# Kernel tuning notes

Hardware: AMD Instinct MI355X
Metric: run time of the kernel (lower is better)

Reference implementation:

```python
import jax, jax.numpy as jnp
import numpy as np

K = 512          # num_embeddings
D = 64           # embedding_dim
BETA = 0.25      # commitment_cost
DECAY = 0.99
EPS = 1e-5


def setup_inputs() -> dict:
    key = jax.random.key(0)
    k1, k2, k3 = jax.random.split(key, 3)
    inputs = jax.random.normal(k1, (64, D, 32, 32), dtype=jnp.float32)  # NCHW, C == embedding_dim
    embedding = jax.random.normal(k2, (K, D), dtype=jnp.float32)
    ema_w = jax.random.normal(k3, (K, D), dtype=jnp.float32)
    ema_cluster_size = jnp.zeros((K,), dtype=jnp.float32)
    return {"inputs": inputs, "embedding": embedding, "ema_w": ema_w,
            "ema_cluster_size": ema_cluster_size}


def reference(inputs, embedding, ema_w, ema_cluster_size):
    # NCHW -> NHWC, flatten to [N, D]
    x = jnp.transpose(inputs, (0, 2, 3, 1))
    B, H, W, C = x.shape
    flat = x.reshape(-1, C)                                   # [N, D]

    # squared L2 distances to all codes: [N, K]
    d = (jnp.sum(flat * flat, axis=1, keepdims=True)
         + jnp.sum(embedding * embedding, axis=1)
         - 2.0 * flat @ embedding.T)
    idx = jnp.argmin(d, axis=1)                               # [N]

    # gather (equivalent to one-hot @ embedding, without materializing one-hot)
    quantized = embedding[idx].reshape(x.shape)               # [B,H,W,D]

    # EMA codebook update (training branch); segment sums replace encodings.T matmuls
    counts = jax.ops.segment_sum(jnp.ones_like(idx, dtype=flat.dtype), idx,
                                 num_segments=K)              # [K]
    new_cs = ema_cluster_size * DECAY + (1.0 - DECAY) * counts
    n = jnp.sum(new_cs)
    new_cs = (new_cs + EPS) / (n + K * EPS) * n               # Laplace smoothing
    dw = jax.ops.segment_sum(flat, idx, num_segments=K)       # [K, D]
    new_ema_w = ema_w * DECAY + (1.0 - DECAY) * dw
    new_embedding = new_ema_w / new_cs[:, None]

    # commitment loss + straight-through estimator
    e_latent_loss = jnp.mean((jax.lax.stop_gradient(quantized) - x) ** 2)
    loss = BETA * e_latent_loss
    quantized_st = x + jax.lax.stop_gradient(quantized - x)

    avg_probs = counts / flat.shape[0]
    perplexity = jnp.exp(-jnp.sum(avg_probs * jnp.log(avg_probs + 1e-10)))

    out_q = jnp.transpose(quantized_st, (0, 3, 1, 2))         # back to NCHW
    return (loss, out_q, perplexity, idx.reshape(B, H, W),
            new_cs, new_ema_w, new_embedding)
```

## Files before the change

kernel.cpp:

```cpp
#include <hip/hip_runtime.h>

#define K_CODES 512
#define DIM 64
#define HW 1024
#define NVEC 65536

#define O0 0
#define O1 1
#define O2 4194305
#define O3 4194306
#define O4 4259842
#define O5 4260354
#define O6 4293122

#define WS_EE  64
#define WS_CNT 1024
#define WS_DW  2048
#define WS_BP  35840
#define XSS    72

typedef __bf16 bf16x8 __attribute__((ext_vector_type(8)));
typedef float  f32x4  __attribute__((ext_vector_type(4)));

__global__ void k0_init(const float* __restrict__ emb, float* __restrict__ wsf) {
    const int b = blockIdx.x, t = threadIdx.x;
    if (b < 128) {
        wsf[WS_DW + b * 256 + t] = 0.0f;
    } else if (b == 128) {
        int* cnt = (int*)(wsf + WS_CNT);
        cnt[t] = 0; cnt[t + 256] = 0;
        if (t == 0) wsf[0] = 0.0f;
    } else if (b < 131) {
        int k = (b - 129) * 256 + t;
        const float* e = emb + k * DIM;
        float s = 0.0f;
        #pragma unroll
        for (int c = 0; c < DIM; ++c) s += e[c] * e[c];
        wsf[WS_EE + k] = s;
    } else {
        int g = (b - 131) * 256 + t;
        int j    = g & 7;
        int lane = (g >> 3) & 63;
        int ks   = (g >> 9) & 1;
        int rest = g >> 10;
        int ntg  = rest & 31;
        int s    = rest >> 5;
        int code = ntg * 16 + (lane & 15);
        int c    = ks * 32 + (lane >> 4) * 8 + j;
        float v = -2.0f * emb[code * DIM + c];
        __bf16 h0 = (__bf16)v;  float r1 = v  - (float)h0;
        __bf16 h1 = (__bf16)r1; float r2 = r1 - (float)h1;
        __bf16 hv = (s == 0) ? h0 : (s == 1 ? h1 : (__bf16)r2);
        ((__bf16*)(wsf + WS_BP))[g] = hv;
    }
}

__global__ __launch_bounds__(512, 2)
void k1_main(const float* __restrict__ in, const float* __restrict__ emb,
             float* __restrict__ out, float* __restrict__ wsf) {
    __shared__ float xs[128 * XSS];
    __shared__ float pmin[4][128];
    __shared__ int   pidx[4][128];
    __shared__ float xxs[128];
    __shared__ int   hist[K_CODES];

    const int t    = threadIdx.x;
    const int lane = t & 63;
    const int wave = t >> 6;
    const int mi2  = wave & 1;
    const int ni2  = wave >> 1;
    const int col  = lane & 15;
    const int quad = lane >> 4;

    hist[t] = 0;

    const int blk     = blockIdx.x;
    const int n_img   = blk >> 3;
    const int hw_base = (blk & 7) * 128;
    const float* xbase = in + n_img * (DIM * HW) + hw_base;

    #pragma unroll
    for (int rep = 0; rep < 16; ++rep) {
        int e = rep * 512 + t;
        int c = e >> 7, h0 = e & 127;
        xs[h0 * XSS + c] = xbase[c * HW + h0];
    }

    f32x4 acc[4][8];
    #pragma unroll
    for (int nt = 0; nt < 8; ++nt) {
        float eev = wsf[WS_EE + ni2 * 128 + nt * 16 + col];
        #pragma unroll
        for (int mi = 0; mi < 4; ++mi) {
            acc[mi][nt][0] = eev; acc[mi][nt][1] = eev;
            acc[mi][nt][2] = eev; acc[mi][nt][3] = eev;
        }
    }

    __syncthreads();

    if (t < 128) {
        float s = 0.0f;
        #pragma unroll
        for (int c = 0; c < DIM; ++c) { float v = xs[t * XSS + c]; s += v * v; }
        xxs[t] = s;
    }

    const bf16x8* bp8 = (const bf16x8*)(wsf + WS_BP);

    #pragma unroll
    for (int ks = 0; ks < 2; ++ks) {
        bf16x8 A0[4], A1[4], A2[4];
        #pragma unroll
        for (int mi = 0; mi < 4; ++mi) {
            const float* src = &xs[(mi2 * 64 + mi * 16 + col) * XSS + ks * 32 + quad * 8];
            #pragma unroll
            for (int j = 0; j < 8; ++j) {
                float v = src[j];
                __bf16 h0 = (__bf16)v;  float r1 = v  - (float)h0;
                __bf16 h1 = (__bf16)r1; float r2 = r1 - (float)h1;
                A0[mi][j] = h0; A1[mi][j] = h1; A2[mi][j] = (__bf16)r2;
            }
        }
        #pragma unroll
        for (int s = 0; s < 3; ++s) {
            bf16x8 Bv[8];
            #pragma unroll
            for (int nt = 0; nt < 8; ++nt)
                Bv[nt] = bp8[(((s * 32 + ni2 * 8 + nt) * 2 + ks) * 64) + lane];
            #pragma unroll
            for (int mi = 0; mi < 4; ++mi)
                #pragma unroll
                for (int nt = 0; nt < 8; ++nt)
                    acc[mi][nt] = __builtin_amdgcn_mfma_f32_16x16x32_bf16(A0[mi], Bv[nt], acc[mi][nt], 0, 0, 0);
            if (s < 2) {
                #pragma unroll
                for (int mi = 0; mi < 4; ++mi)
                    #pragma unroll
                    for (int nt = 0; nt < 8; ++nt)
                        acc[mi][nt] = __builtin_amdgcn_mfma_f32_16x16x32_bf16(A1[mi], Bv[nt], acc[mi][nt], 0, 0, 0);
            }
            if (s == 0) {
                #pragma unroll
                for (int mi = 0; mi < 4; ++mi)
                    #pragma unroll
                    for (int nt = 0; nt < 8; ++nt)
                        acc[mi][nt] = __builtin_amdgcn_mfma_f32_16x16x32_bf16(A2[mi], Bv[nt], acc[mi][nt], 0, 0, 0);
            }
        }
    }

    #pragma unroll
    for (int mi = 0; mi < 4; ++mi) {
        #pragma unroll
        for (int r = 0; r < 4; ++r) {
            float v  = acc[mi][0][r];
            int   bi = ni2 * 128 + col;
            #pragma unroll
            for (int nt = 1; nt < 8; ++nt) {
                float u  = acc[mi][nt][r];
                int   ui = ni2 * 128 + nt * 16 + col;
                if (u < v) { v = u; bi = ui; }
            }
            #pragma unroll
            for (int off = 1; off < 16; off <<= 1) {
                float ov = __shfl_xor(v, off);
                int   oi = __shfl_xor(bi, off);
                if (ov < v || (ov == v && oi < bi)) { v = ov; bi = oi; }
            }
            if (col == 0) {
                int row = mi2 * 64 + mi * 16 + quad * 4 + r;
                pmin[ni2][row] = v;
                pidx[ni2][row] = bi;
            }
        }
    }
    __syncthreads();

    if (t < 128) {
        float v = pmin[0][t]; int bi = pidx[0][t];
        #pragma unroll
        for (int q = 1; q < 4; ++q) {
            float u = pmin[q][t]; int ui = pidx[q][t];
            if (u < v) { v = u; bi = ui; }
        }
        pidx[0][t] = bi;
        out[O3 + blk * 128 + t] = (float)bi;
        atomicAdd(&hist[bi], 1);
        float ld = v + xxs[t];
        #pragma unroll
        for (int off = 32; off > 0; off >>= 1) ld += __shfl_down(ld, off);
        if ((t & 63) == 0) atomicAdd(wsf + 0, ld);
    }
    __syncthreads();

    {
        int v = t & 127, cq = t >> 7;
        int kv = pidx[0][v];
        const float* ew = emb + kv * DIM;
        float* oq = out + O1 + n_img * (DIM * HW) + hw_base + v;
        #pragma unroll
        for (int c = cq * 16; c < cq * 16 + 16; ++c) oq[c * HW] = ew[c];
    }

    {
        float* dw = wsf + WS_DW;
        #pragma unroll 1
        for (int v = wave * 16; v < wave * 16 + 16; ++v) {
            int kv = pidx[0][v];
            atomicAdd(&dw[kv * DIM + lane], xs[v * XSS + lane]);
        }
    }

    int* cnt = (int*)(wsf + WS_CNT);
    if (hist[t]) atomicAdd(&cnt[t], hist[t]);
}

__global__ void k2a(const float* __restrict__ ema_cs, float* __restrict__ out,
                    const float* __restrict__ wsf) {
    __shared__ float s1[512], s2[512];
    const int t = threadIdx.x;
    const int* cnt = (const int*)(wsf + WS_CNT);
    float c   = (float)cnt[t];
    float raw = 0.99f * ema_cs[t] + 0.01f * c;
    float p   = c * (1.0f / 65536.0f);
    s1[t] = raw;
    s2[t] = p * logf(p + 1e-10f);
    __syncthreads();
    for (int s = 256; s > 0; s >>= 1) {
        if (t < s) { s1[t] += s1[t + s]; s2[t] += s2[t + s]; }
        __syncthreads();
    }
    float n = s1[0];
    float smooth = (raw + 1e-5f) / (n + 512.0f * 1e-5f) * n;
    out[O4 + t] = smooth;
    if (t == 0) {
        out[O2] = expf(-s2[0]);
        out[O0] = 0.25f * wsf[0] * (1.0f / 4194304.0f);
    }
}

__global__ void k2b(const float* __restrict__ ema_w, const float* __restrict__ wsf,
                    float* __restrict__ out) {
    const int m = blockIdx.x * 256 + threadIdx.x;
    const int k = m >> 6;
    float w = 0.99f * ema_w[m] + 0.01f * wsf[WS_DW + m];
    out[O5 + m] = w;
    out[O6 + m] = w / out[O4 + k];
}

extern "C" void kernel_launch(void* const* d_in, const int* in_sizes, int n_in,
                              void* d_out, int out_size, void* d_ws, size_t ws_size,
                              hipStream_t stream) {
    const float* in     = (const float*)d_in[0];
    const float* emb    = (const float*)d_in[1];
    const float* ema_w  = (const float*)d_in[2];
    const float* ema_cs = (const float*)d_in[3];
    float* out = (float*)d_out;
    float* wsf = (float*)d_ws;

    hipLaunchKernelGGL(k0_init, dim3(515), dim3(256), 0, stream, emb, wsf);
    hipLaunchKernelGGL(k1_main, dim3(512), dim3(512), 0, stream, in, emb, out, wsf);
    hipLaunchKernelGGL(k2a,     dim3(1),   dim3(512), 0, stream, ema_cs, out, wsf);
    hipLaunchKernelGGL(k2b,     dim3(128), dim3(256), 0, stream, ema_w, wsf, out);
}
```

Baseline: 161.2 us.

## Replicate atomic accumulators, write per-block loss partials, fuse finalize kernels

Splits the dw and count accumulators into four replicas indexed by block, so atomics from different blocks land on different copies and contend less. Each block writes its loss partial to its own slot instead of doing a global float atomic. The two finalize kernels are merged into one 128-block kernel that sums the replicas and recomputes the smoothed cluster sizes per block, which drops one launch. In exchange the init kernel zeroes four times as much workspace and the finalize does more redundant reads.

```diff
diff --git a/kernel.cpp b/kernel.cpp
--- a/kernel.cpp
+++ b/kernel.cpp
@@ -4,6 +4,7 @@
 #define DIM 64
 #define HW 1024
 #define NVEC 65536
+#define NREP 4
 
 #define O0 0
 #define O1 1
@@ -13,32 +14,33 @@
 #define O5 4260354
 #define O6 4293122
 
-#define WS_EE  64
-#define WS_CNT 1024
-#define WS_DW  2048
-#define WS_BP  35840
-#define XSS    72
+#define WS_LOSS 0
+#define WS_EE   512
+#define WS_CNT  1024
+#define WS_DW   4096
+#define WS_BP   135168
+#define XSS     72
 
 typedef __bf16 bf16x8 __attribute__((ext_vector_type(8)));
 typedef float  f32x4  __attribute__((ext_vector_type(4)));
 
 __global__ void k0_init(const float* __restrict__ emb, float* __restrict__ wsf) {
     const int b = blockIdx.x, t = threadIdx.x;
-    if (b < 128) {
+    if (b < 512) {
         wsf[WS_DW + b * 256 + t] = 0.0f;
-    } else if (b == 128) {
+    } else if (b == 512) {
         int* cnt = (int*)(wsf + WS_CNT);
-        cnt[t] = 0; cnt[t + 256] = 0;
-        if (t == 0) wsf[0] = 0.0f;
-    } else if (b < 131) {
-        int k = (b - 129) * 256 + t;
+        #pragma unroll
+        for (int i = 0; i < 8; ++i) cnt[i * 256 + t] = 0;
+    } else if (b < 515) {
+        int k = (b - 513) * 256 + t;
         const float* e = emb + k * DIM;
         float s = 0.0f;
         #pragma unroll
         for (int c = 0; c < DIM; ++c) s += e[c] * e[c];
         wsf[WS_EE + k] = s;
     } else {
-        int g = (b - 131) * 256 + t;
+        int g = (b - 515) * 256 + t;
         int j    = g & 7;
         int lane = (g >> 3) & 63;
         int ks   = (g >> 9) & 1;
@@ -62,6 +64,7 @@
     __shared__ float pmin[4][128];
     __shared__ int   pidx[4][128];
     __shared__ float xxs[128];
+    __shared__ float lsum[2];
     __shared__ int   hist[K_CODES];
 
     const int t    = threadIdx.x;
@@ -75,13 +78,14 @@
     hist[t] = 0;
 
     const int blk     = blockIdx.x;
+    const int rep     = blk & (NREP - 1);
     const int n_img   = blk >> 3;
     const int hw_base = (blk & 7) * 128;
     const float* xbase = in + n_img * (DIM * HW) + hw_base;
 
     #pragma unroll
-    for (int rep = 0; rep < 16; ++rep) {
-        int e = rep * 512 + t;
+    for (int rp = 0; rp < 16; ++rp) {
+        int e = rp * 512 + t;
         int c = e >> 7, h0 = e & 127;
         xs[h0 * XSS + c] = xbase[c * HW + h0];
     }
@@ -190,9 +194,11 @@
         float ld = v + xxs[t];
         #pragma unroll
         for (int off = 32; off > 0; off >>= 1) ld += __shfl_down(ld, off);
-        if ((t & 63) == 0) atomicAdd(wsf + 0, ld);
-    }
-    __syncthreads();
+        if ((t & 63) == 0) lsum[t >> 6] = ld;
+    }
+    __syncthreads();
+
+    if (t == 0) wsf[WS_LOSS + blk] = lsum[0] + lsum[1];
 
     {
         int v = t & 127, cq = t >> 7;
@@ -204,7 +210,7 @@
     }
 
     {
-        float* dw = wsf + WS_DW;
+        float* dw = wsf + WS_DW + rep * 32768;
         #pragma unroll 1
         for (int v = wave * 16; v < wave * 16 + 16; ++v) {
             int kv = pidx[0][v];
@@ -213,40 +219,67 @@
     }
 
     int* cnt = (int*)(wsf + WS_CNT);
-    if (hist[t]) atomicAdd(&cnt[t], hist[t]);
-}
-
-__global__ void k2a(const float* __restrict__ ema_cs, float* __restrict__ out,
-                    const float* __restrict__ wsf) {
-    __shared__ float s1[512], s2[512];
+    if (hist[t]) atomicAdd(&cnt[rep * 512 + t], hist[t]);
+}
+
+__global__ void k2(const float* __restrict__ ema_cs, const float* __restrict__ ema_w,
+                   float* __restrict__ out, const float* __restrict__ wsf) {
+    __shared__ float s1[256], s2[256];
     const int t = threadIdx.x;
+    const int blk = blockIdx.x;
     const int* cnt = (const int*)(wsf + WS_CNT);
-    float c   = (float)cnt[t];
-    float raw = 0.99f * ema_cs[t] + 0.01f * c;
-    float p   = c * (1.0f / 65536.0f);
-    s1[t] = raw;
-    s2[t] = p * logf(p + 1e-10f);
-    __syncthreads();
-    for (int s = 256; s > 0; s >>= 1) {
+
+    float ca = 0.0f, cb = 0.0f;
+    #pragma unroll
+    for (int r = 0; r < NREP; ++r) {
+        ca += (float)cnt[r * 512 + t];
+        cb += (float)cnt[r * 512 + 256 + t];
+    }
+    float ra = 0.99f * ema_cs[t]       + 0.01f * ca;
+    float rb = 0.99f * ema_cs[256 + t] + 0.01f * cb;
+    float pa = ca * (1.0f / 65536.0f);
+    float pb = cb * (1.0f / 65536.0f);
+    s1[t] = ra + rb;
+    s2[t] = pa * logf(pa + 1e-10f) + pb * logf(pb + 1e-10f);
+    __syncthreads();
+    for (int s = 128; s > 0; s >>= 1) {
         if (t < s) { s1[t] += s1[t + s]; s2[t] += s2[t + s]; }
         __syncthreads();
     }
-    float n = s1[0];
-    float smooth = (raw + 1e-5f) / (n + 512.0f * 1e-5f) * n;
-    out[O4 + t] = smooth;
-    if (t == 0) {
-        out[O2] = expf(-s2[0]);
-        out[O0] = 0.25f * wsf[0] * (1.0f / 4194304.0f);
-    }
-}
-
-__global__ void k2b(const float* __restrict__ ema_w, const float* __restrict__ wsf,
-                    float* __restrict__ out) {
-    const int m = blockIdx.x * 256 + threadIdx.x;
-    const int k = m >> 6;
-    float w = 0.99f * ema_w[m] + 0.01f * wsf[WS_DW + m];
-    out[O5 + m] = w;
-    out[O6 + m] = w / out[O4 + k];
+    const float n = s1[0];
+    const float den = n + 512.0f * 1e-5f;
+
+    {
+        int m = blk * 256 + t;
+        int k = m >> 6;
+        float dwsum = wsf[WS_DW + m] + wsf[WS_DW + 32768 + m]
+                    + wsf[WS_DW + 65536 + m] + wsf[WS_DW + 98304 + m];
+        float w = 0.99f * ema_w[m] + 0.01f * dwsum;
+        float ck = 0.0f;
+        #pragma unroll
+        for (int r = 0; r < NREP; ++r) ck += (float)cnt[r * 512 + k];
+        float rawk = 0.99f * ema_cs[k] + 0.01f * ck;
+        float csk = (rawk + 1e-5f) / den * n;
+        out[O5 + m] = w;
+        out[O6 + m] = w / csk;
+    }
+
+    if (blk == 0) {
+        float s2v = s2[0];
+        out[O4 + t]       = (ra + 1e-5f) / den * n;
+        out[O4 + 256 + t] = (rb + 1e-5f) / den * n;
+        __syncthreads();
+        s1[t] = wsf[WS_LOSS + t] + wsf[WS_LOSS + 256 + t];
+        __syncthreads();
+        for (int s = 128; s > 0; s >>= 1) {
+            if (t < s) s1[t] += s1[t + s];
+            __syncthreads();
+        }
+        if (t == 0) {
+            out[O0] = 0.25f * s1[0] * (1.0f / 4194304.0f);
+            out[O2] = expf(-s2v);
+        }
+    }
 }
 
 extern "C" void kernel_launch(void* const* d_in, const int* in_sizes, int n_in,
@@ -259,8 +292,7 @@
     float* out = (float*)d_out;
     float* wsf = (float*)d_ws;
 
-    hipLaunchKernelGGL(k0_init, dim3(515), dim3(256), 0, stream, emb, wsf);
+    hipLaunchKernelGGL(k0_init, dim3(899), dim3(256), 0, stream, emb, wsf);
     hipLaunchKernelGGL(k1_main, dim3(512), dim3(512), 0, stream, in, emb, out, wsf);
-    hipLaunchKernelGGL(k2a,     dim3(1),   dim3(512), 0, stream, ema_cs, out, wsf);
-    hipLaunchKernelGGL(k2b,     dim3(128), dim3(256), 0, stream, ema_w, wsf, out);
-}
+    hipLaunchKernelGGL(k2,      dim3(128), dim3(256), 0, stream, ema_cs, ema_w, out, wsf);
+}
```

Result: faster. 147.7 us (-8.4%).
